# Performance work log

Measured on AMD Instinct MI355X. Metric: run time of the kernel, lower is better.

The kernel has to match this reference:

```python
import jax, jax.numpy as jnp
import numpy as np

B, T, E, H = 2, 2048, 2048, 16
D = E // H  # head dim = 128
ROPE_BASE = 10000.0


def setup_inputs() -> dict:
    key = jax.random.key(0)
    ks = jax.random.split(key, 9)
    s = 1.0 / np.sqrt(E)
    return {
        "x": jax.random.normal(ks[0], (B, T, E), jnp.float32),
        "Wq": jax.random.normal(ks[1], (E, E), jnp.float32) * s,
        "bq": jax.random.normal(ks[2], (E,), jnp.float32) * s,
        "Wk": jax.random.normal(ks[3], (E, E), jnp.float32) * s,
        "bk": jax.random.normal(ks[4], (E,), jnp.float32) * s,
        "Wv": jax.random.normal(ks[5], (E, E), jnp.float32) * s,
        "bv": jax.random.normal(ks[6], (E,), jnp.float32) * s,
        "Wo": jax.random.normal(ks[7], (E, E), jnp.float32) * s,
        "bo": jax.random.normal(ks[8], (E,), jnp.float32) * s,
    }


def _rope(x):
    # x: [b, h, t, d]; positions are 1-indexed (m+1) as in the source
    t, d = x.shape[-2], x.shape[-1]
    j = jnp.arange(d // 2, dtype=x.dtype)
    thetas = ROPE_BASE ** (-2.0 * j / d)                  # [d/2]
    m = jnp.arange(1, t + 1, dtype=x.dtype)               # [t]
    ang = m[:, None] * thetas[None, :]                    # [t, d/2]
    C = jnp.concatenate([ang, ang], axis=-1)              # [t, d]
    x_rot = jnp.concatenate([-x[..., d // 2:], x[..., :d // 2]], axis=-1)
    return x * jnp.cos(C) + x_rot * jnp.sin(C)


def reference(x, Wq, bq, Wk, bk, Wv, bv, Wo, bo):
    b, t, e = x.shape
    # projections (nn.Linear: x @ W.T + b)
    def proj(W, bias):
        y = jnp.einsum('bte,fe->btf', x, W) + bias
        return y.reshape(b, t, H, D).transpose(0, 2, 1, 3)  # b h t d
    q = _rope(proj(Wq, bq))
    k = _rope(proj(Wk, bk))
    v = proj(Wv, bv)

    scale = jnp.sqrt(jnp.asarray(D, x.dtype))
    att = jnp.einsum('bhqd,bhkd->bhqk', q, k) / scale
    causal = jnp.tril(jnp.ones((t, t), bool))
    att = jnp.where(causal, att, -jnp.inf)
    att = jax.nn.softmax(att, axis=-1)
    y = jnp.einsum('bhqk,bhkd->bhqd', att, v)
    y = y.transpose(0, 2, 1, 3).reshape(b, t, e)
    y = jnp.einsum('bte,fe->btf', y, Wo) + bo
    return y
```

## Files before the change

### kernel.cpp

```cpp
#include <hip/hip_runtime.h>
#include <hip/hip_bf16.h>

typedef __bf16 bf16_t;
typedef __bf16 bf16x4 __attribute__((ext_vector_type(4)));
typedef __bf16 bf16x8 __attribute__((ext_vector_type(8)));
typedef float  f32x4  __attribute__((ext_vector_type(4)));

#define GLD_LDS16(gptr, lptr)                                                        \
    __builtin_amdgcn_global_load_lds((__attribute__((address_space(1))) void*)(gptr),\
                                     (__attribute__((address_space(3))) void*)(lptr),\
                                     16, 0, 0)

constexpr int Bc = 2, Tc = 2048, Ec = 2048, Hc = 16, Dc = 128;
constexpr int Mtok = Bc * Tc;

__device__ __forceinline__ bf16x8 cvt8(const float* p) {
    f32x4 a = *(const f32x4*)p;
    f32x4 b = *(const f32x4*)(p + 4);
    bf16x8 r;
    r[0] = (bf16_t)a[0]; r[1] = (bf16_t)a[1];
    r[2] = (bf16_t)a[2]; r[3] = (bf16_t)a[3];
    r[4] = (bf16_t)b[0]; r[5] = (bf16_t)b[1];
    r[6] = (bf16_t)b[2]; r[7] = (bf16_t)b[3];
    return r;
}

__global__ void convert_bf16(const float* __restrict__ src, bf16_t* __restrict__ dst) {
    size_t i = ((size_t)blockIdx.x * 256 + threadIdx.x) * 8;
    *(bf16x8*)&dst[i] = cvt8(src + i);
}

__global__ void convert_w(const float* __restrict__ Wq, const float* __restrict__ Wk,
                          const float* __restrict__ Wv, const float* __restrict__ Wo,
                          bf16_t* __restrict__ w4) {
    int blk = blockIdx.x;
    int wi  = blk >> 11;
    const float* src = (wi == 0) ? Wq : (wi == 1) ? Wk : (wi == 2) ? Wv : Wo;
    bf16_t* dst = w4 + (size_t)wi * Ec * Ec;
    size_t i = ((size_t)(blk & 2047) * 256 + threadIdx.x) * 8;
    *(bf16x8*)&dst[i] = cvt8(src + i);
}

__global__ __launch_bounds__(512, 2) void gemm_qkv_z(const bf16_t* __restrict__ A,
                                                     const bf16_t* __restrict__ w3,
                                                     const float* __restrict__ bq,
                                                     const float* __restrict__ bk,
                                                     const float* __restrict__ bv,
                                                     bf16_t* __restrict__ qo,
                                                     bf16_t* __restrict__ ko,
                                                     bf16_t* __restrict__ vto) {
    __shared__ __align__(16) bf16_t ldsA[3 * 8192];
    __shared__ __align__(16) bf16_t ldsB[3 * 12288];

    const int tid  = threadIdx.x;
    const int wave = tid >> 6;
    const int lane = tid & 63;
    const int g    = lane >> 4;
    const int n16  = lane & 15;
    const int wm   = wave >> 2;
    const int wn   = wave & 3;
    const int m0   = blockIdx.x * 256;
    const int n0   = blockIdx.y * 384;
    const int K    = Ec;

    const int sr   = tid >> 2;
    const int scol = (((tid & 3) ^ ((tid >> 3) & 3)) << 3);
    const bf16_t* srcA = A  + (size_t)(m0 + sr) * K + scol;
    const bf16_t* srcB = w3 + (size_t)(n0 + sr) * K + scol;
    const int dwave = wave * 512;

    const int fsw = (n16 >> 1) & 3;

    constexpr int NT = Ec / 32;

#define STG_A2(jj, buf)                                                         \
    do { if ((jj) < NT) {                                                       \
        const bf16_t* _s = srcA + (jj) * 32;                                    \
        bf16_t* _d = &ldsA[(buf) * 8192 + dwave];                               \
        GLD_LDS16(_s, _d);                                                      \
        GLD_LDS16(_s + (size_t)128 * K, _d + 4096);                             \
    } } while (0)
#define STG_B1(jj, buf)                                                         \
    do { if ((jj) < NT) {                                                       \
        GLD_LDS16(srcB + (jj) * 32, &ldsB[(buf) * 12288 + dwave]);              \
    } } while (0)
#define STG_B2(jj, buf)                                                         \
    do { if ((jj) < NT) {                                                       \
        const bf16_t* _s = srcB + (jj) * 32;                                    \
        bf16_t* _d = &ldsB[(buf) * 12288 + dwave];                              \
        GLD_LDS16(_s + (size_t)128 * K, _d + 4096);                             \
        GLD_LDS16(_s + (size_t)256 * K, _d + 8192);                             \
    } } while (0)

    f32x4 acc[8][6] = {};
    bf16x8 af[4], af2[4], bfr[6];

    STG_A2(0, 0); STG_B1(0, 0); STG_B2(0, 0);
    STG_A2(1, 1); STG_B1(1, 1); STG_B2(1, 1);
    asm volatile("s_waitcnt vmcnt(5)" ::: "memory");
    __builtin_amdgcn_s_barrier();
    asm volatile("" ::: "memory");

    int bc = 0;
    int bi = 2;
#pragma unroll 1
    for (int j = 0; j < NT; ++j) {
        const bf16_t* la = &ldsA[bc * 8192];
        const bf16_t* lb = &ldsB[bc * 12288];

#pragma unroll
        for (int mt = 0; mt < 4; ++mt)
            af[mt] = *(const bf16x8*)&la[(wm * 128 + mt * 16 + n16) * 32 +
                                         ((g ^ fsw) << 3)];
#pragma unroll
        for (int l = 0; l < 6; ++l)
            bfr[l] = *(const bf16x8*)&lb[(wn * 96 + l * 16 + n16) * 32 +
                                         ((g ^ fsw) << 3)];
        STG_A2(j + 2, bi);
        STG_B1(j + 2, bi);
        asm volatile("s_waitcnt lgkmcnt(0)" ::: "memory");
        __builtin_amdgcn_sched_barrier(0);
        __builtin_amdgcn_s_setprio(1);
#pragma unroll
        for (int mt = 0; mt < 4; ++mt)
#pragma unroll
            for (int l = 0; l < 6; ++l)
                acc[mt][l] = __builtin_amdgcn_mfma_f32_16x16x32_bf16(
                    af[mt], bfr[l], acc[mt][l], 0, 0, 0);
        __builtin_amdgcn_s_setprio(0);
        __builtin_amdgcn_s_barrier();
        asm volatile("" ::: "memory");

#pragma unroll
        for (int mt = 0; mt < 4; ++mt)
            af2[mt] = *(const bf16x8*)&la[(wm * 128 + 64 + mt * 16 + n16) * 32 +
                                          ((g ^ fsw) << 3)];
        STG_B2(j + 2, bi);
        asm volatile("s_waitcnt lgkmcnt(0)" ::: "memory");
        __builtin_amdgcn_sched_barrier(0);
        __builtin_amdgcn_s_setprio(1);
#pragma unroll
        for (int mt = 0; mt < 4; ++mt)
#pragma unroll
            for (int l = 0; l < 6; ++l)
                acc[4 + mt][l] = __builtin_amdgcn_mfma_f32_16x16x32_bf16(
                    af2[mt], bfr[l], acc[4 + mt][l], 0, 0, 0);
        __builtin_amdgcn_s_setprio(0);

        if (j < NT - 2)      { asm volatile("s_waitcnt vmcnt(5)" ::: "memory"); }
        else if (j < NT - 1) { asm volatile("s_waitcnt vmcnt(0)" ::: "memory"); }
        __builtin_amdgcn_s_barrier();
        asm volatile("" ::: "memory");

        bc = (bc == 2) ? 0 : bc + 1;
        bi = (bi == 2) ? 0 : bi + 1;
    }
#undef STG_A2
#undef STG_B1
#undef STG_B2

#pragma unroll
    for (int l = 0; l < 6; ++l) {
        int n   = n0 + wn * 96 + l * 16 + n16;
        int mat = n >> 11;
        int nn  = n & 2047;
        const float* bp = (mat == 0) ? bq : (mat == 1) ? bk : bv;
        float bn = bp[nn];
        int h = nn >> 7, d = nn & (Dc - 1);
#pragma unroll
        for (int i = 0; i < 8; ++i) {
            int mb = m0 + wm * 128 + (i >> 2) * 64 + (i & 3) * 16 + g * 4;
            int b = mb >> 11, t = mb & (Tc - 1);
            if (mat == 2) {
                bf16x4 pk;
#pragma unroll
                for (int r = 0; r < 4; ++r) pk[r] = (bf16_t)(acc[i][l][r] + bn);
                *(bf16x4*)&vto[(((size_t)(b * Hc + h)) * Dc + d) * Tc + t] = pk;
            } else {
                bf16_t* outb = (mat == 0) ? qo : ko;
#pragma unroll
                for (int r = 0; r < 4; ++r)
                    outb[(((size_t)(b * Hc + h)) * Tc + (t + r)) * Dc + d] =
                        (bf16_t)(acc[i][l][r] + bn);
            }
        }
    }
}

__global__ __launch_bounds__(512, 2) void gemm_out_p(const bf16_t* __restrict__ A,
                                                     const bf16_t* __restrict__ W,
                                                     const float* __restrict__ bias,
                                                     float* __restrict__ out) {
    __shared__ __align__(16) bf16_t ldsA[3 * 256 * 32];
    __shared__ __align__(16) bf16_t ldsB[3 * 128 * 32];

    const int tid  = threadIdx.x;
    const int wave = tid >> 6;
    const int lane = tid & 63;
    const int g    = lane >> 4;
    const int n16  = lane & 15;
    const int wm   = wave >> 1;
    const int wn   = wave & 1;
    const int m0   = blockIdx.x * 256;
    const int n0   = blockIdx.y * 128;
    const int K    = Ec;

    const int sr   = tid >> 2;
    const int scol = (((tid & 3) ^ ((tid >> 3) & 3)) << 3);
    const bf16_t* gA0 = A + (size_t)(m0 + sr) * K + scol;
    const bf16_t* gA1 = A + (size_t)(m0 + 128 + sr) * K + scol;
    const bf16_t* gB  = W + (size_t)(n0 + sr) * K + scol;
    const int dL = wave * 512;

    const int fsw = (n16 >> 1) & 3;
    const int rAo = (wm * 64 + n16) * 32 + ((g ^ fsw) << 3);
    const int rBo = (wn * 64 + n16) * 32 + ((g ^ fsw) << 3);

    f32x4 acc[4][4] = {};

    constexpr int NT = Ec / 32;
#pragma unroll
    for (int tt = 0; tt < 2; ++tt) {
        GLD_LDS16(gA0 + tt * 32, &ldsA[tt * 8192 + dL]);
        GLD_LDS16(gA1 + tt * 32, &ldsA[tt * 8192 + 4096 + dL]);
        GLD_LDS16(gB  + tt * 32, &ldsB[tt * 4096 + dL]);
    }

    int bc = 0, bi = 2;
#pragma unroll 1
    for (int t = 0; t < NT; ++t) {
        if (t < NT - 1) { asm volatile("s_waitcnt vmcnt(3)" ::: "memory"); }
        else            { asm volatile("s_waitcnt vmcnt(0)" ::: "memory"); }
        __builtin_amdgcn_s_barrier();
        asm volatile("" ::: "memory");

        const bf16_t* la = &ldsA[bc * 8192];
        const bf16_t* lb = &ldsB[bc * 4096];
        bf16x8 af[4], bfr[4];
#pragma unroll
        for (int mt = 0; mt < 4; ++mt) af[mt] = *(const bf16x8*)&la[rAo + mt * 512];
#pragma unroll
        for (int nt = 0; nt < 4; ++nt) bfr[nt] = *(const bf16x8*)&lb[rBo + nt * 512];

        if (t + 2 < NT) {
            GLD_LDS16(gA0 + (t + 2) * 32, &ldsA[bi * 8192 + dL]);
            GLD_LDS16(gA1 + (t + 2) * 32, &ldsA[bi * 8192 + 4096 + dL]);
            GLD_LDS16(gB  + (t + 2) * 32, &ldsB[bi * 4096 + dL]);
        }

        asm volatile("s_waitcnt lgkmcnt(0)" ::: "memory");
        __builtin_amdgcn_sched_barrier(0);
        __builtin_amdgcn_s_setprio(1);
#pragma unroll
        for (int mt = 0; mt < 4; ++mt)
#pragma unroll
            for (int nt = 0; nt < 4; ++nt)
                acc[mt][nt] = __builtin_amdgcn_mfma_f32_16x16x32_bf16(
                    af[mt], bfr[nt], acc[mt][nt], 0, 0, 0);
        __builtin_amdgcn_s_setprio(0);

        bc = (bc == 2) ? 0 : bc + 1;
        bi = (bi == 2) ? 0 : bi + 1;
    }

    const int row_off = wm * 64;
    const int col_off = wn * 64;
#pragma unroll
    for (int nt = 0; nt < 4; ++nt) {
        int n = n0 + col_off + nt * 16 + n16;
        float bn = bias[n];
#pragma unroll
        for (int mt = 0; mt < 4; ++mt) {
            int mb = m0 + row_off + mt * 16 + g * 4;
#pragma unroll
            for (int r = 0; r < 4; ++r)
                out[(size_t)(mb + r) * Ec + n] = acc[mt][nt][r] + bn;
        }
    }
}

__global__ __launch_bounds__(256) void gemm_qkv(const bf16_t* __restrict__ A,
                                                const float* __restrict__ Wq,
                                                const float* __restrict__ Wk,
                                                const float* __restrict__ Wv,
                                                const float* __restrict__ bq,
                                                const float* __restrict__ bk,
                                                const float* __restrict__ bv,
                                                bf16_t* __restrict__ qo,
                                                bf16_t* __restrict__ ko,
                                                bf16_t* __restrict__ vto) {
    __shared__ __align__(16) bf16_t ldsA[128 * 32];
    __shared__ __align__(16) bf16_t ldsB[128 * 32];

    const int tid  = threadIdx.x;
    const int wave = tid >> 6;
    const int lane = tid & 63;
    const int g    = lane >> 4;
    const int n16  = lane & 15;
    const int m0   = blockIdx.x * 128;
    const int mat  = blockIdx.y >> 4;
    const int n0   = (blockIdx.y & 15) * 128;
    const int row_off = (wave >> 1) * 64;
    const int col_off = (wave & 1) * 64;
    const int K = Ec;

    const float* W    = (mat == 0) ? Wq : (mat == 1) ? Wk : Wv;
    const float* bias = (mat == 0) ? bq : (mat == 1) ? bk : bv;

    f32x4 acc[4][4] = {};

    const int r0 = tid >> 2;
    const int cc = tid & 3;
    const size_t a0 = (size_t)(m0 + r0) * K + cc * 8;
    const size_t a1 = (size_t)(m0 + r0 + 64) * K + cc * 8;
    const float* pb0 = W + (size_t)(n0 + r0) * K + cc * 8;
    const float* pb1 = W + (size_t)(n0 + r0 + 64) * K + cc * 8;

    for (int k0 = 0; k0 < K; k0 += 32) {
        bf16x8 vb0 = cvt8(pb0 + k0);
        bf16x8 vb1 = cvt8(pb1 + k0);
        __syncthreads();
        GLD_LDS16(A + a0 + k0, &ldsA[(wave * 64) * 8]);
        GLD_LDS16(A + a1 + k0, &ldsA[(256 + wave * 64) * 8]);
        *(bf16x8*)&ldsB[(size_t)tid * 8]         = vb0;
        *(bf16x8*)&ldsB[(size_t)(256 + tid) * 8] = vb1;
        __syncthreads();

        bf16x8 af[4], bfr[4];
#pragma unroll
        for (int mt = 0; mt < 4; ++mt)
            af[mt] = *(const bf16x8*)&ldsA[(row_off + mt * 16 + n16) * 32 + g * 8];
#pragma unroll
        for (int nt = 0; nt < 4; ++nt)
            bfr[nt] = *(const bf16x8*)&ldsB[(col_off + nt * 16 + n16) * 32 + g * 8];
#pragma unroll
        for (int mt = 0; mt < 4; ++mt)
#pragma unroll
            for (int nt = 0; nt < 4; ++nt)
                acc[mt][nt] = __builtin_amdgcn_mfma_f32_16x16x32_bf16(
                    af[mt], bfr[nt], acc[mt][nt], 0, 0, 0);
    }

#pragma unroll
    for (int nt = 0; nt < 4; ++nt) {
        int n = n0 + col_off + nt * 16 + n16;
        float bn = bias[n];
        int h = n >> 7, d = n & (Dc - 1);
#pragma unroll
        for (int mt = 0; mt < 4; ++mt) {
            int mb = m0 + row_off + mt * 16 + g * 4;
            int b = mb >> 11, t = mb & (Tc - 1);
            if (mat == 2) {
                bf16x4 pk;
#pragma unroll
                for (int r = 0; r < 4; ++r) pk[r] = (bf16_t)(acc[mt][nt][r] + bn);
                *(bf16x4*)&vto[(((size_t)(b * Hc + h)) * Dc + d) * Tc + t] = pk;
            } else {
                bf16_t* outb = (mat == 0) ? qo : ko;
#pragma unroll
                for (int r = 0; r < 4; ++r)
                    outb[(((size_t)(b * Hc + h)) * Tc + (t + r)) * Dc + d] =
                        (bf16_t)(acc[mt][nt][r] + bn);
            }
        }
    }
}

__global__ __launch_bounds__(256) void gemm_out(const bf16_t* __restrict__ A,
                                                const float* __restrict__ W,
                                                const float* __restrict__ bias,
                                                float* __restrict__ out,
                                                int M, int N, int K) {
    __shared__ __align__(16) bf16_t ldsA[128 * 32];
    __shared__ __align__(16) bf16_t ldsB[128 * 32];

    const int tid  = threadIdx.x;
    const int wave = tid >> 6;
    const int lane = tid & 63;
    const int g    = lane >> 4;
    const int n16  = lane & 15;
    const int m0 = blockIdx.x * 128;
    const int n0 = blockIdx.y * 128;
    const int row_off = (wave >> 1) * 64;
    const int col_off = (wave & 1) * 64;

    f32x4 acc[4][4] = {};

    const int r0 = tid >> 2;
    const int cc = tid & 3;
    const size_t a0 = (size_t)(m0 + r0) * K + cc * 8;
    const size_t a1 = (size_t)(m0 + r0 + 64) * K + cc * 8;
    const float* pb0 = W + (size_t)(n0 + r0) * K + cc * 8;
    const float* pb1 = W + (size_t)(n0 + r0 + 64) * K + cc * 8;

    for (int k0 = 0; k0 < K; k0 += 32) {
        bf16x8 vb0 = cvt8(pb0 + k0);
        bf16x8 vb1 = cvt8(pb1 + k0);
        __syncthreads();
        GLD_LDS16(A + a0 + k0, &ldsA[(wave * 64) * 8]);
        GLD_LDS16(A + a1 + k0, &ldsA[(256 + wave * 64) * 8]);
        *(bf16x8*)&ldsB[(size_t)tid * 8]         = vb0;
        *(bf16x8*)&ldsB[(size_t)(256 + tid) * 8] = vb1;
        __syncthreads();

        bf16x8 af[4], bfr[4];
#pragma unroll
        for (int mt = 0; mt < 4; ++mt)
            af[mt] = *(const bf16x8*)&ldsA[(row_off + mt * 16 + n16) * 32 + g * 8];
#pragma unroll
        for (int nt = 0; nt < 4; ++nt)
            bfr[nt] = *(const bf16x8*)&ldsB[(col_off + nt * 16 + n16) * 32 + g * 8];
#pragma unroll
        for (int mt = 0; mt < 4; ++mt)
#pragma unroll
            for (int nt = 0; nt < 4; ++nt)
                acc[mt][nt] = __builtin_amdgcn_mfma_f32_16x16x32_bf16(
                    af[mt], bfr[nt], acc[mt][nt], 0, 0, 0);
    }

#pragma unroll
    for (int nt = 0; nt < 4; ++nt) {
        int n = n0 + col_off + nt * 16 + n16;
        float bn = bias[n];
#pragma unroll
        for (int mt = 0; mt < 4; ++mt) {
            int mb = m0 + row_off + mt * 16 + g * 4;
#pragma unroll
            for (int r = 0; r < 4; ++r)
                out[(size_t)(mb + r) * N + n] = acc[mt][nt][r] + bn;
        }
    }
}

__global__ void rope_kernel(bf16_t* __restrict__ q, bf16_t* __restrict__ k) {
    int row = blockIdx.x * 4 + (threadIdx.x >> 6);
    int d   = threadIdx.x & 63;
    int t   = row & (Tc - 1);
    float theta = powf(10000.0f, -(float)d * (1.0f / 64.0f));
    float ang   = (float)(t + 1) * theta;
    float sv, cv;
    sincosf(ang, &sv, &cv);
    size_t base = (size_t)row * Dc;
    float q1 = (float)q[base + d], q2 = (float)q[base + d + 64];
    q[base + d]      = (bf16_t)(q1 * cv - q2 * sv);
    q[base + d + 64] = (bf16_t)(q2 * cv + q1 * sv);
    float k1 = (float)k[base + d], k2 = (float)k[base + d + 64];
    k[base + d]      = (bf16_t)(k1 * cv - k2 * sv);
    k[base + d + 64] = (bf16_t)(k2 * cv + k1 * sv);
}

constexpr int KP = 128 + 8;
constexpr int VP = 64 + 8;
constexpr int PP = 64 + 8;

__global__ __launch_bounds__(256) void attn_kernel(const bf16_t* __restrict__ q,
                                                   const bf16_t* __restrict__ kmat,
                                                   const bf16_t* __restrict__ vt,
                                                   bf16_t* __restrict__ out) {
    __shared__ __align__(16) bf16_t k_lds[64 * KP];
    __shared__ __align__(16) bf16_t v_lds[128 * VP];
    __shared__ __align__(16) bf16_t p_lds[4 * 16 * PP];

    const int tid  = threadIdx.x;
    const int wave = tid >> 6, lane = tid & 63;
    const int g = lane >> 4, n16 = lane & 15;
    const int pi = blockIdx.x;
    const int bh = blockIdx.y;
    const size_t base = (size_t)bh * Tc * Dc;
    const int b = bh >> 4, h = bh & 15;
    const float sc2 = 0.08838834764831845f * 1.4426950408889634f;
    bf16_t* pw = &p_lds[wave * 16 * PP];

    const int kr_key = tid >> 4, kr_c = tid & 15;
    const int vr_dd  = tid >> 3, vr_c = tid & 7;

#pragma unroll 1
    for (int half = 0; half < 2; ++half) {
        const int qt = half ? pi : 31 - pi;
        const int q0 = qt * 64;

        bf16x8 qf[4];
        {
            const bf16_t* qp = q + base + (size_t)(q0 + wave * 16 + n16) * Dc + g * 8;
#pragma unroll
            for (int kk = 0; kk < 4; ++kk) qf[kk] = *(const bf16x8*)(qp + kk * 32);
        }

        float m_run[4], l_run[4];
#pragma unroll
        for (int r = 0; r < 4; ++r) { m_run[r] = -1e30f; l_run[r] = 0.0f; }
        f32x4 o_acc[8] = {};

        bf16x8 rk[4], rv[4];
#pragma unroll
        for (int i = 0; i < 4; ++i)
            rk[i] = *(const bf16x8*)&kmat[base + (size_t)(i * 16 + kr_key) * Dc + kr_c * 8];
#pragma unroll
        for (int i = 0; i < 4; ++i)
            rv[i] = *(const bf16x8*)&vt[base + (size_t)(i * 32 + vr_dd) * Tc + vr_c * 8];

#pragma unroll 1
        for (int kt = 0; kt <= qt; ++kt) {
            const int k0 = kt * 64;
            __syncthreads();
#pragma unroll
            for (int i = 0; i < 4; ++i)
                *(bf16x8*)&k_lds[(i * 16 + kr_key) * KP + kr_c * 8] = rk[i];
#pragma unroll
            for (int i = 0; i < 4; ++i)
                *(bf16x8*)&v_lds[(i * 32 + vr_dd) * VP + vr_c * 8] = rv[i];
            __syncthreads();

            if (kt < qt) {
                const int kn = k0 + 64;
#pragma unroll
                for (int i = 0; i < 4; ++i)
                    rk[i] = *(const bf16x8*)&kmat[base + (size_t)(kn + i * 16 + kr_key) * Dc + kr_c * 8];
#pragma unroll
                for (int i = 0; i < 4; ++i)
                    rv[i] = *(const bf16x8*)&vt[base + (size_t)(i * 32 + vr_dd) * Tc + kn + vr_c * 8];
            }

            f32x4 s_acc[4];
#pragma unroll
            for (int nt = 0; nt < 4; ++nt) {
                f32x4 a = {};
                int key = nt * 16 + n16;
#pragma unroll
                for (int kk = 0; kk < 4; ++kk) {
                    bf16x8 kf = *(const bf16x8*)&k_lds[key * KP + kk * 32 + g * 8];
                    a = __builtin_amdgcn_mfma_f32_16x16x32_bf16(qf[kk], kf, a, 0, 0, 0);
                }
                s_acc[nt] = a;
            }

            if (kt == qt) {
#pragma unroll
                for (int nt = 0; nt < 4; ++nt) {
                    int key = k0 + nt * 16 + n16;
#pragma unroll
                    for (int r = 0; r < 4; ++r) {
                        int qq = q0 + wave * 16 + g * 4 + r;
                        float v = s_acc[nt][r] * sc2;
                        s_acc[nt][r] = (key <= qq) ? v : -1e30f;
                    }
                }
            } else {
#pragma unroll
                for (int nt = 0; nt < 4; ++nt)
#pragma unroll
                    for (int r = 0; r < 4; ++r) s_acc[nt][r] *= sc2;
            }

            float alpha[4];
#pragma unroll
            for (int r = 0; r < 4; ++r) {
                float rm = fmaxf(fmaxf(s_acc[0][r], s_acc[1][r]),
                                 fmaxf(s_acc[2][r], s_acc[3][r]));
                rm = fmaxf(rm, __shfl_xor(rm, 1, 16));
                rm = fmaxf(rm, __shfl_xor(rm, 2, 16));
                rm = fmaxf(rm, __shfl_xor(rm, 4, 16));
                rm = fmaxf(rm, __shfl_xor(rm, 8, 16));
                float m_new = fmaxf(m_run[r], rm);
                alpha[r] = __builtin_amdgcn_exp2f(m_run[r] - m_new);
                m_run[r] = m_new;
                float sum = 0.0f;
#pragma unroll
                for (int nt = 0; nt < 4; ++nt) {
                    float p = __builtin_amdgcn_exp2f(s_acc[nt][r] - m_new);
                    s_acc[nt][r] = p;
                    sum += p;
                }
                l_run[r] = l_run[r] * alpha[r] + sum;
            }
#pragma unroll
            for (int dt = 0; dt < 8; ++dt)
#pragma unroll
                for (int r = 0; r < 4; ++r) o_acc[dt][r] *= alpha[r];

#pragma unroll
            for (int nt = 0; nt < 4; ++nt) {
                int key = nt * 16 + n16;
#pragma unroll
                for (int r = 0; r < 4; ++r)
                    pw[(g * 4 + r) * PP + key] = (bf16_t)s_acc[nt][r];
            }
            bf16x8 pf[2];
#pragma unroll
            for (int kk = 0; kk < 2; ++kk)
                pf[kk] = *(const bf16x8*)&pw[n16 * PP + kk * 32 + g * 8];

#pragma unroll
            for (int dt = 0; dt < 8; ++dt) {
                int dd = dt * 16 + n16;
#pragma unroll
                for (int kk = 0; kk < 2; ++kk) {
                    bf16x8 vf = *(const bf16x8*)&v_lds[dd * VP + kk * 32 + g * 8];
                    o_acc[dt] = __builtin_amdgcn_mfma_f32_16x16x32_bf16(
                        pf[kk], vf, o_acc[dt], 0, 0, 0);
                }
            }
        }

        float inv_l[4];
#pragma unroll
        for (int r = 0; r < 4; ++r) {
            float s = l_run[r];
            s += __shfl_xor(s, 1, 16);
            s += __shfl_xor(s, 2, 16);
            s += __shfl_xor(s, 4, 16);
            s += __shfl_xor(s, 8, 16);
            inv_l[r] = 1.0f / s;
        }
#pragma unroll
        for (int dt = 0; dt < 8; ++dt) {
            int d = dt * 16 + n16;
#pragma unroll
            for (int r = 0; r < 4; ++r) {
                int qq = q0 + wave * 16 + g * 4 + r;
                out[((size_t)(b * Tc + qq)) * Ec + h * Dc + d] =
                    (bf16_t)(o_acc[dt][r] * inv_l[r]);
            }
        }
    }
}

extern "C" void kernel_launch(void* const* d_in, const int* in_sizes, int n_in,
                              void* d_out, int out_size, void* d_ws, size_t ws_size,
                              hipStream_t stream) {
    const float* x  = (const float*)d_in[0];
    const float* Wq = (const float*)d_in[1];
    const float* bq = (const float*)d_in[2];
    const float* Wk = (const float*)d_in[3];
    const float* bk = (const float*)d_in[4];
    const float* Wv = (const float*)d_in[5];
    const float* bv = (const float*)d_in[6];
    const float* Wo = (const float*)d_in[7];
    const float* bo = (const float*)d_in[8];
    float* out = (float*)d_out;

    char* ws = (char*)d_ws;
    const size_t sz  = (size_t)Bc * Hc * Tc * Dc * sizeof(bf16_t);
    const size_t szW = (size_t)Ec * Ec * sizeof(bf16_t);
    bf16_t* q   = (bf16_t*)(ws);
    bf16_t* k   = (bf16_t*)(ws + sz);
    bf16_t* vt  = (bf16_t*)(ws + 2 * sz);
    bf16_t* xb  = (bf16_t*)(ws + 3 * sz);
    bf16_t* att = xb;

    if (ws_size >= 4 * sz + 4 * szW) {
        bf16_t* w4 = (bf16_t*)(ws + 4 * sz);
        convert_bf16<<<Mtok * Ec / (256 * 8), 256, 0, stream>>>(x, xb);
        convert_w<<<8192, 256, 0, stream>>>(Wq, Wk, Wv, Wo, w4);
        gemm_qkv_z<<<dim3(Mtok / 256, 16), 512, 0, stream>>>(xb, w4, bq, bk, bv,
                                                             q, k, vt);
        rope_kernel<<<Bc * Hc * Tc / 4, 256, 0, stream>>>(q, k);
        attn_kernel<<<dim3(16, Bc * Hc), 256, 0, stream>>>(q, k, vt, att);
        gemm_out_p<<<dim3(Mtok / 256, Ec / 128), 512, 0, stream>>>(
            att, w4 + 3 * (size_t)Ec * Ec, bo, out);
    } else {
        convert_bf16<<<Mtok * Ec / (256 * 8), 256, 0, stream>>>(x, xb);
        gemm_qkv<<<dim3(Mtok / 128, 48), 256, 0, stream>>>(xb, Wq, Wk, Wv,
                                                           bq, bk, bv, q, k, vt);
        rope_kernel<<<Bc * Hc * Tc / 4, 256, 0, stream>>>(q, k);
        attn_kernel<<<dim3(16, Bc * Hc), 256, 0, stream>>>(q, k, vt, att);
        gemm_out<<<dim3(Mtok / 128, Ec / 128), 256, 0, stream>>>(att, Wo, bo, out,
                                                                 Mtok, Ec, Ec);
    }
}
```

Baseline: 395.9 us.

## Fold softmax scale into RoPE of Q and skip lazy rescale in attention

Pre-multiplies Q by the softmax scale times log2(e) inside the RoPE kernel, which removes the per-score multiply in attention. Adds a lazy online-softmax rescale: when every row's new max stays within 8 (log2 units) of the running max, the alpha computation and the rescale of the output accumulator are skipped. Also sets a minimum occupancy of 3 blocks in launch bounds. The risks are extra bf16 rounding on the scaled Q, possibly larger exponent values, and register pressure from the occupancy hint.

```diff
diff --git a/kernel.cpp b/kernel.cpp
--- a/kernel.cpp
+++ b/kernel.cpp
@@ -436,14 +436,15 @@
     int row = blockIdx.x * 4 + (threadIdx.x >> 6);
     int d   = threadIdx.x & 63;
     int t   = row & (Tc - 1);
+    const float sc2 = 0.08838834764831845f * 1.4426950408889634f;
     float theta = powf(10000.0f, -(float)d * (1.0f / 64.0f));
     float ang   = (float)(t + 1) * theta;
     float sv, cv;
     sincosf(ang, &sv, &cv);
     size_t base = (size_t)row * Dc;
     float q1 = (float)q[base + d], q2 = (float)q[base + d + 64];
-    q[base + d]      = (bf16_t)(q1 * cv - q2 * sv);
-    q[base + d + 64] = (bf16_t)(q2 * cv + q1 * sv);
+    q[base + d]      = (bf16_t)((q1 * cv - q2 * sv) * sc2);
+    q[base + d + 64] = (bf16_t)((q2 * cv + q1 * sv) * sc2);
     float k1 = (float)k[base + d], k2 = (float)k[base + d + 64];
     k[base + d]      = (bf16_t)(k1 * cv - k2 * sv);
     k[base + d + 64] = (bf16_t)(k2 * cv + k1 * sv);
@@ -453,10 +454,10 @@
 constexpr int VP = 64 + 8;
 constexpr int PP = 64 + 8;
 
-__global__ __launch_bounds__(256) void attn_kernel(const bf16_t* __restrict__ q,
-                                                   const bf16_t* __restrict__ kmat,
-                                                   const bf16_t* __restrict__ vt,
-                                                   bf16_t* __restrict__ out) {
+__global__ __launch_bounds__(256, 3) void attn_kernel(const bf16_t* __restrict__ q,
+                                                      const bf16_t* __restrict__ kmat,
+                                                      const bf16_t* __restrict__ vt,
+                                                      bf16_t* __restrict__ out) {
     __shared__ __align__(16) bf16_t k_lds[64 * KP];
     __shared__ __align__(16) bf16_t v_lds[128 * VP];
     __shared__ __align__(16) bf16_t p_lds[4 * 16 * PP];
@@ -468,7 +469,6 @@
     const int bh = blockIdx.y;
     const size_t base = (size_t)bh * Tc * Dc;
     const int b = bh >> 4, h = bh & 15;
-    const float sc2 = 0.08838834764831845f * 1.4426950408889634f;
     bf16_t* pw = &p_lds[wave * 16 * PP];
 
     const int kr_key = tid >> 4, kr_c = tid & 15;
@@ -541,18 +541,13 @@
 #pragma unroll
                     for (int r = 0; r < 4; ++r) {
                         int qq = q0 + wave * 16 + g * 4 + r;
-                        float v = s_acc[nt][r] * sc2;
-                        s_acc[nt][r] = (key <= qq) ? v : -1e30f;
+                        if (key > qq) s_acc[nt][r] = -1e30f;
                     }
                 }
-            } else {
-#pragma unroll
-                for (int nt = 0; nt < 4; ++nt)
-#pragma unroll
-                    for (int r = 0; r < 4; ++r) s_acc[nt][r] *= sc2;
-            }
-
-            float alpha[4];
+            }
+
+            float rm4[4];
+            int ok = 1;
 #pragma unroll
             for (int r = 0; r < 4; ++r) {
                 float rm = fmaxf(fmaxf(s_acc[0][r], s_acc[1][r]),
@@ -561,22 +556,42 @@
                 rm = fmaxf(rm, __shfl_xor(rm, 2, 16));
                 rm = fmaxf(rm, __shfl_xor(rm, 4, 16));
                 rm = fmaxf(rm, __shfl_xor(rm, 8, 16));
-                float m_new = fmaxf(m_run[r], rm);
-                alpha[r] = __builtin_amdgcn_exp2f(m_run[r] - m_new);
-                m_run[r] = m_new;
-                float sum = 0.0f;
-#pragma unroll
-                for (int nt = 0; nt < 4; ++nt) {
-                    float p = __builtin_amdgcn_exp2f(s_acc[nt][r] - m_new);
-                    s_acc[nt][r] = p;
-                    sum += p;
+                rm4[r] = rm;
+                ok &= (rm <= m_run[r] + 8.0f);
+            }
+            if (__all(ok)) {
+#pragma unroll
+                for (int r = 0; r < 4; ++r) {
+                    float sum = 0.0f;
+#pragma unroll
+                    for (int nt = 0; nt < 4; ++nt) {
+                        float p = __builtin_amdgcn_exp2f(s_acc[nt][r] - m_run[r]);
+                        s_acc[nt][r] = p;
+                        sum += p;
+                    }
+                    l_run[r] += sum;
                 }
-                l_run[r] = l_run[r] * alpha[r] + sum;
-            }
-#pragma unroll
-            for (int dt = 0; dt < 8; ++dt)
-#pragma unroll
-                for (int r = 0; r < 4; ++r) o_acc[dt][r] *= alpha[r];
+            } else {
+                float alpha[4];
+#pragma unroll
+                for (int r = 0; r < 4; ++r) {
+                    float m_new = fmaxf(m_run[r], rm4[r]);
+                    alpha[r] = __builtin_amdgcn_exp2f(m_run[r] - m_new);
+                    m_run[r] = m_new;
+                    float sum = 0.0f;
+#pragma unroll
+                    for (int nt = 0; nt < 4; ++nt) {
+                        float p = __builtin_amdgcn_exp2f(s_acc[nt][r] - m_new);
+                        s_acc[nt][r] = p;
+                        sum += p;
+                    }
+                    l_run[r] = l_run[r] * alpha[r] + sum;
+                }
+#pragma unroll
+                for (int dt = 0; dt < 8; ++dt)
+#pragma unroll
+                    for (int r = 0; r < 4; ++r) o_acc[dt][r] *= alpha[r];
+            }
 
 #pragma unroll
             for (int nt = 0; nt < 4; ++nt) {
```

Result: slower. 462.8 us (+16.9%).
